# Optimization experiments

Measured on AMD Instinct MI355X. Metric: run time of the kernel, lower is better.

## Reference

```python
import jax, jax.numpy as jnp
import numpy as np

B, N, D = 64, 512, 256
IMG = 51  # hard-coded image-token prefix length from the original forward
EPS = 1e-8


def _l2norm(x):
    # matches torch.cosine_similarity eps clamping on each vector norm
    n = jnp.linalg.norm(x, axis=-1, keepdims=True)
    return x / jnp.maximum(n, EPS)


def setup_inputs() -> dict:
    key = jax.random.key(0)
    ks = jax.random.split(key, 10)
    s = 1.0 / np.sqrt(D)
    return {
        "input_1": jax.random.normal(ks[0], (B, N, D), jnp.float32),
        "input_2": jax.random.normal(ks[1], (B, N, D), jnp.float32),
        "attention_mask": jnp.ones((B, N), jnp.int32),  # unused by forward, kept for signature fidelity
        "noun_mask": jax.random.randint(ks[2], (B, N), 0, 2, jnp.int32),
        "w0": jax.random.uniform(ks[3], (D, D), jnp.float32, -s, s),
        "b0": jax.random.uniform(ks[4], (D,), jnp.float32, -s, s),
        "w1": jax.random.uniform(ks[5], (D, D), jnp.float32, -s, s),
        "b1": jax.random.uniform(ks[6], (D,), jnp.float32, -s, s),
        "wf": jax.random.uniform(ks[7], (D, D), jnp.float32, -s, s),
        "bf": jax.random.uniform(ks[8], (D,), jnp.float32, -s, s),
    }


def reference(input_1, input_2, attention_mask, noun_mask, w0, b0, w1, b1, wf, bf):
    img = _l2norm(input_2[:, :IMG, :])    # [B, 51, D]
    text = _l2norm(input_2[:, IMG:, :])   # [B, N-51, D]
    # cosine similarity via normalized matmul (no O(N*M*D) repeat blowup)
    sim = jnp.einsum('bid,btd->bit', img, text)            # [B, 51, N-51]
    nm = noun_mask[:, IMG:].astype(sim.dtype)[:, None, :]  # [B, 1, N-51]
    sim = sim * nm
    text_sim = jnp.einsum('bid,bjd->bij', text, text)      # [B, N-51, N-51]
    adj = jnp.zeros((B, N, N), input_2.dtype)
    adj = adj.at[:, :IMG, IMG:].set(sim)
    adj = adj.at[:, IMG:, :IMG].set(jnp.swapaxes(sim, 1, 2))
    adj = adj.at[:, IMG:, IMG:].set(text_sim)
    h = input_1
    for w, b in ((w0, b0), (w1, b1)):  # gcn_layer_num = 2; dropout is identity at eval
        h = jax.nn.relu(jnp.einsum('bnm,bmd->bnd', adj, h) @ w.T + b)
    return jax.nn.relu(h @ wf.T + bf)
```

## Files before the change

kernel.cpp:

```cpp
#include <hip/hip_runtime.h>
#include <math.h>

#define Bn   64
#define Nn   512
#define Dn   256
#define IMGn 51

typedef __attribute__((ext_vector_type(8))) short bf16x8;
typedef __attribute__((ext_vector_type(4))) float f32x4;
typedef __attribute__((ext_vector_type(4))) unsigned short u16x4;

__device__ inline unsigned short f2b(float f) {
    union { float f; unsigned u; } v; v.f = f;
    unsigned r = v.u + 0x7fffu + ((v.u >> 16) & 1u);
    return (unsigned short)(r >> 16);
}

__global__ __launch_bounds__(256) void k_prep(const float* __restrict__ in1,
                                              const float* __restrict__ in2,
                                              const float* __restrict__ w0,
                                              const float* __restrict__ w1,
                                              const float* __restrict__ wf,
                                              unsigned short* __restrict__ A0,
                                              unsigned short* __restrict__ T,
                                              unsigned short* __restrict__ w0b,
                                              unsigned short* __restrict__ w1b,
                                              unsigned short* __restrict__ wfb) {
    const int bid = blockIdx.x, tid = threadIdx.x;
    if (bid < 8192) {
        const int xcd = bid & 7, j = bid >> 3;
        const int b = xcd * 8 + (j >> 7), rb = j & 127;
        const int row = b * 512 + rb * 4 + (tid >> 6);
        const int lane = tid & 63;
        float4 v = ((const float4*)(in2 + (size_t)row * Dn))[lane];
        float ss = v.x * v.x + v.y * v.y + v.z * v.z + v.w * v.w;
#pragma unroll
        for (int m = 1; m < 64; m <<= 1) ss += __shfl_xor(ss, m);
        float inv = 1.0f / fmaxf(sqrtf(ss), 1e-8f);
        u16x4 o = { f2b(v.x*inv), f2b(v.y*inv), f2b(v.z*inv), f2b(v.w*inv) };
        ((u16x4*)(T + (size_t)row * Dn))[lane] = o;
    } else if (bid < 10240) {
        const int id2 = bid - 8192;
        const int xcd = id2 & 7, j = id2 >> 3;
        const int b = xcd * 8 + (j >> 5), jj = j & 31;
        int i = b * 32768 + jj * 1024 + tid;
#pragma unroll
        for (int q = 0; q < 4; ++q, i += 256) {
            float4 v = ((const float4*)in1)[i];
            u16x4 o = { f2b(v.x), f2b(v.y), f2b(v.z), f2b(v.w) };
            ((u16x4*)A0)[i] = o;
        }
    } else {
        const int b2 = bid - 10240;
        const float* src = (b2 < 64) ? w0 : (b2 < 128) ? w1 : wf;
        unsigned short* dst = (b2 < 64) ? w0b : (b2 < 128) ? w1b : wfb;
        const int i = (b2 & 63) * 256 + tid;
        float4 v = ((const float4*)src)[i];
        u16x4 o = { f2b(v.x), f2b(v.y), f2b(v.z), f2b(v.w) };
        ((u16x4*)dst)[i] = o;
    }
}

__device__ inline void stage128x32(const unsigned short* __restrict__ src, int ldk,
                                   char* ldsbase, int tid) {
    const int wave = tid >> 6, lane = tid & 63;
#pragma unroll
    for (int it = 0; it < 2; ++it) {
        const int chunk = wave * 128 + it * 64 + lane;
        const int row = chunk >> 2, s = chunk & 3;
        const char* g = (const char*)(src + (size_t)row * ldk) + ((s ^ ((row >> 1) & 3)) << 4);
        char* l = ldsbase + (size_t)(wave * 2048 + it * 1024);
        __builtin_amdgcn_global_load_lds((const __attribute__((address_space(1))) void*)g,
                                         (__attribute__((address_space(3))) void*)l,
                                         16, 0, 0);
    }
}

__device__ inline bf16x8 frag(const char* ldsbase, int row, int s) {
    return *(const bf16x8*)(ldsbase + row * 64 + ((s ^ ((row >> 1) & 3)) << 4));
}

__device__ inline void gemm_loop(const unsigned short* __restrict__ A,
                                 const unsigned short* __restrict__ Bt,
                                 int lda, int ldb, int NT, char* smem, int tid,
                                 int wr, int wc, int r16, int s, f32x4 (&acc)[4][4]) {
#pragma unroll
    for (int m = 0; m < 4; ++m)
#pragma unroll
        for (int n = 0; n < 4; ++n) acc[m][n] = (f32x4){0.f, 0.f, 0.f, 0.f};
    stage128x32(A,  lda, smem,        tid);
    stage128x32(Bt, ldb, smem + 8192, tid);
    __syncthreads();
    for (int t = 0; t < NT; ++t) {
        if (t + 1 < NT) {
            char* nb = smem + 17408 * ((t + 1) & 1);
            stage128x32(A  + (t + 1) * 32, lda, nb,        tid);
            stage128x32(Bt + (t + 1) * 32, ldb, nb + 8192, tid);
        }
        const char* cb = smem + 17408 * (t & 1);
        bf16x8 af[4], bv[4];
#pragma unroll
        for (int m = 0; m < 4; ++m) af[m] = frag(cb,        wr * 64 + m * 16 + r16, s);
#pragma unroll
        for (int n = 0; n < 4; ++n) bv[n] = frag(cb + 8192, wc * 64 + n * 16 + r16, s);
#pragma unroll
        for (int m = 0; m < 4; ++m)
#pragma unroll
            for (int n = 0; n < 4; ++n)
                acc[m][n] = __builtin_amdgcn_mfma_f32_16x16x32_bf16(af[m], bv[n], acc[m][n], 0, 0, 0);
        __syncthreads();
    }
}

__global__ __launch_bounds__(256, 4) void k_gt(const unsigned short* __restrict__ T_,
                                               const unsigned short* __restrict__ A0,
                                               const unsigned short* __restrict__ w0b,
                                               const int* __restrict__ noun,
                                               unsigned short* __restrict__ adj,
                                               unsigned short* __restrict__ Ut) {
    __shared__ char smem[34816];
    const int tid = threadIdx.x, lane = tid & 63, wave = tid >> 6;
    const int wr = wave >> 1, wc = wave & 1;
    const int r16 = lane & 15, s = lane >> 4;
    const int id = blockIdx.x, xcd = id & 7, gid = id >> 3;
    f32x4 acc[4][4];

    if (gid < 80) {
        const int b = xcd * 8 + (gid & 7);
        const int tile = gid >> 3;
        int ty_, tx_;
        if (tile < 4)      { ty_ = 0; tx_ = tile; }
        else if (tile < 7) { ty_ = 1; tx_ = tile - 3; }
        else if (tile < 9) { ty_ = 2; tx_ = tile - 5; }
        else               { ty_ = 3; tx_ = 3; }
        const unsigned short* Tb = T_ + (size_t)b * Nn * Dn;
        gemm_loop(Tb + (size_t)ty_ * 128 * Dn, Tb + (size_t)tx_ * 128 * Dn,
                  Dn, Dn, 8, smem, tid, wr, wc, r16, s, acc);
        const int row0 = ty_ * 128, col0 = tx_ * 128;
        const int* nm = noun + b * Nn;
        unsigned short* out = adj + (size_t)b * Nn * Nn;
        unsigned short* lt = (unsigned short*)smem;
        const int row = tid >> 1, h = tid & 1;
#pragma unroll
        for (int n = 0; n < 4; ++n) {
            const int cl = wc * 64 + n * 16 + r16;
            const int c  = col0 + cl;
            const float nmc = (c < IMGn) ? 0.f : (float)nm[c];
#pragma unroll
            for (int m = 0; m < 4; ++m)
#pragma unroll
                for (int i = 0; i < 4; ++i) {
                    const int rl = wr * 64 + m * 16 + s * 4 + i;
                    const int r  = row0 + rl;
                    float mask;
                    if (r < IMGn)      mask = nmc;
                    else if (c < IMGn) mask = (float)nm[r];
                    else               mask = 1.f;
                    lt[rl * 136 + cl] = f2b(acc[m][n][i] * mask);
                }
        }
        __syncthreads();
        {
            const bf16x8* srcv = (const bf16x8*)(lt + (size_t)row * 136 + h * 64);
            bf16x8* dstv = (bf16x8*)(out + (size_t)(row0 + row) * Nn + col0 + h * 64);
#pragma unroll
            for (int q = 0; q < 8; ++q) dstv[q] = srcv[q];
        }
        if (tx_ != ty_) {
            __syncthreads();
#pragma unroll
            for (int n = 0; n < 4; ++n) {
                const int cl = wc * 64 + n * 16 + r16;
                const int c  = col0 + cl;
                const float nmc = (c < IMGn) ? 0.f : (float)nm[c];
#pragma unroll
                for (int m = 0; m < 4; ++m)
#pragma unroll
                    for (int i = 0; i < 4; ++i) {
                        const int rl = wr * 64 + m * 16 + s * 4 + i;
                        const int r  = row0 + rl;
                        float mask;
                        if (r < IMGn)      mask = nmc;
                        else if (c < IMGn) mask = (float)nm[r];
                        else               mask = 1.f;
                        lt[cl * 136 + rl] = f2b(acc[m][n][i] * mask);
                    }
            }
            __syncthreads();
            const bf16x8* srcv = (const bf16x8*)(lt + (size_t)row * 136 + h * 64);
            bf16x8* dstv = (bf16x8*)(out + (size_t)(col0 + row) * Nn + row0 + h * 64);
#pragma unroll
            for (int q = 0; q < 8; ++q) dstv[q] = srcv[q];
        }
    } else {
        const int idx = xcd * 64 + (gid - 80);
        const int tx = idx & 1, ty = idx >> 1;
        gemm_loop(A0 + (size_t)ty * 128 * Dn, w0b + (size_t)tx * 128 * Dn,
                  Dn, Dn, 8, smem, tid, wr, wc, r16, s, acc);
        unsigned short* lt = (unsigned short*)smem;
#pragma unroll
        for (int n = 0; n < 4; ++n)
#pragma unroll
            for (int m = 0; m < 4; ++m)
#pragma unroll
                for (int i = 0; i < 4; ++i) {
                    const int ct = wc * 64 + n * 16 + r16;
                    const int rt = wr * 64 + m * 16 + s * 4 + i;
                    lt[ct * 136 + rt] = f2b(acc[m][n][i]);
                }
        __syncthreads();
        const size_t bb = ty >> 2;
        const int rl0 = (ty & 3) * 128, col0 = tx * 128;
        unsigned short* out = Ut + bb * ((size_t)Dn * Nn);
        const int ct = tid >> 1, h = tid & 1;
        const bf16x8* srcv = (const bf16x8*)(lt + (size_t)ct * 136 + h * 64);
        bf16x8* dstv = (bf16x8*)(out + (size_t)(col0 + ct) * Nn + rl0 + h * 64);
#pragma unroll
        for (int q = 0; q < 8; ++q) dstv[q] = srcv[q];
    }
}

__global__ __launch_bounds__(256, 4) void k_biash(const unsigned short* __restrict__ adj,
                                                  const unsigned short* __restrict__ Ut,
                                                  const float* __restrict__ bias,
                                                  unsigned short* __restrict__ H) {
    __shared__ char smem[34816];
    const int tid = threadIdx.x, lane = tid & 63, wave = tid >> 6;
    const int wr = wave >> 1, wc = wave & 1;
    const int r16 = lane & 15, s = lane >> 4;
    const int id = blockIdx.x, xcd = id & 7, gid = id >> 3;
    const int b = xcd * 8 + (gid >> 3);
    const int tile = gid & 7, tx = tile & 1, ty = tile >> 1;
    f32x4 acc[4][4];
    gemm_loop(adj + (size_t)b * Nn * Nn + (size_t)ty * 128 * Nn,
              Ut  + (size_t)b * Dn * Nn + (size_t)tx * 128 * Nn,
              Nn, Nn, 16, smem, tid, wr, wc, r16, s, acc);
    const int row0 = ty * 128, col0 = tx * 128;
    unsigned short* lt = (unsigned short*)smem;
#pragma unroll
    for (int n = 0; n < 4; ++n) {
        const int cl = wc * 64 + n * 16 + r16;
        const float bvv = bias[col0 + cl];
#pragma unroll
        for (int m = 0; m < 4; ++m)
#pragma unroll
            for (int i = 0; i < 4; ++i) {
                const int rl = wr * 64 + m * 16 + s * 4 + i;
                lt[rl * 136 + cl] = f2b(fmaxf(acc[m][n][i] + bvv, 0.f));
            }
    }
    __syncthreads();
    unsigned short* out = H + (size_t)b * Nn * Dn;
    const int row = tid >> 1, h = tid & 1;
    const bf16x8* srcv = (const bf16x8*)(lt + (size_t)row * 136 + h * 64);
    bf16x8* dstv = (bf16x8*)(out + (size_t)(row0 + row) * Dn + col0 + h * 64);
#pragma unroll
    for (int q = 0; q < 8; ++q) dstv[q] = srcv[q];
}

__global__ __launch_bounds__(256, 4) void k_trans(const unsigned short* __restrict__ Hin,
                                                  const unsigned short* __restrict__ Wb,
                                                  unsigned short* __restrict__ Ut) {
    __shared__ char smem[34816];
    const int tid = threadIdx.x, lane = tid & 63, wave = tid >> 6;
    const int wr = wave >> 1, wc = wave & 1;
    const int r16 = lane & 15, s = lane >> 4;
    const int id = blockIdx.x, xcd = id & 7;
    const int idx = xcd * 64 + (id >> 3);
    const int tx = idx & 1, ty = idx >> 1;
    f32x4 acc[4][4];
    gemm_loop(Hin + (size_t)ty * 128 * Dn, Wb + (size_t)tx * 128 * Dn,
              Dn, Dn, 8, smem, tid, wr, wc, r16, s, acc);
    unsigned short* lt = (unsigned short*)smem;
#pragma unroll
    for (int n = 0; n < 4; ++n)
#pragma unroll
        for (int m = 0; m < 4; ++m)
#pragma unroll
            for (int i = 0; i < 4; ++i) {
                const int ct = wc * 64 + n * 16 + r16;
                const int rt = wr * 64 + m * 16 + s * 4 + i;
                lt[ct * 136 + rt] = f2b(acc[m][n][i]);
            }
    __syncthreads();
    const size_t bb = ty >> 2;
    const int rl0 = (ty & 3) * 128, col0 = tx * 128;
    unsigned short* out = Ut + bb * ((size_t)Dn * Nn);
    const int ct = tid >> 1, h = tid & 1;
    const bf16x8* srcv = (const bf16x8*)(lt + (size_t)ct * 136 + h * 64);
    bf16x8* dstv = (bf16x8*)(out + (size_t)(col0 + ct) * Nn + rl0 + h * 64);
#pragma unroll
    for (int q = 0; q < 8; ++q) dstv[q] = srcv[q];
}

__global__ __launch_bounds__(256, 4) void k_final(const unsigned short* __restrict__ H2,
                                                  const unsigned short* __restrict__ wfb,
                                                  const float* __restrict__ bias,
                                                  float* __restrict__ out) {
    __shared__ char smem[34816];
    const int tid = threadIdx.x, lane = tid & 63, wave = tid >> 6;
    const int wr = wave >> 1, wc = wave & 1;
    const int r16 = lane & 15, s = lane >> 4;
    const int id = blockIdx.x, xcd = id & 7;
    const int idx = xcd * 64 + (id >> 3);
    const int tx = idx & 1, ty = idx >> 1;
    f32x4 acc[4][4];
    gemm_loop(H2 + (size_t)ty * 128 * Dn, wfb + (size_t)tx * 128 * Dn,
              Dn, Dn, 8, smem, tid, wr, wc, r16, s, acc);
    const int row0 = ty * 128, col0 = tx * 128;
    float* lt32 = (float*)smem;
    const int row = tid >> 1, h = tid & 1;
#pragma unroll
    for (int p = 0; p < 2; ++p) {
        if (p) __syncthreads();
        if (wc == p) {
#pragma unroll
            for (int n = 0; n < 4; ++n) {
                const int cll = n * 16 + r16;
                const float bvv = bias[col0 + p * 64 + cll];
#pragma unroll
                for (int m = 0; m < 4; ++m)
#pragma unroll
                    for (int i = 0; i < 4; ++i) {
                        const int rl = wr * 64 + m * 16 + s * 4 + i;
                        lt32[rl * 68 + cll] = fmaxf(acc[m][n][i] + bvv, 0.f);
                    }
            }
        }
        __syncthreads();
        const float4* srcv = (const float4*)(lt32 + (size_t)row * 68 + h * 32);
        float4* dstv = (float4*)(out + (size_t)(row0 + row) * Dn + col0 + p * 64 + h * 32);
#pragma unroll
        for (int q = 0; q < 8; ++q) dstv[q] = srcv[q];
    }
}

extern "C" void kernel_launch(void* const* d_in, const int* in_sizes, int n_in,
                              void* d_out, int out_size, void* d_ws, size_t ws_size,
                              hipStream_t stream) {
    const float* input_1 = (const float*)d_in[0];
    const float* input_2 = (const float*)d_in[1];
    const int*   noun    = (const int*)d_in[3];
    const float* w0 = (const float*)d_in[4];
    const float* b0 = (const float*)d_in[5];
    const float* w1 = (const float*)d_in[6];
    const float* b1 = (const float*)d_in[7];
    const float* wf = (const float*)d_in[8];
    const float* bf = (const float*)d_in[9];

    unsigned short* ws  = (unsigned short*)d_ws;
    unsigned short* T   = ws;
    unsigned short* A0  = ws +  8388608;
    unsigned short* adj = ws + 16777216;
    unsigned short* Ut  = ws + 33554432;
    unsigned short* H1  = ws + 41943040;
    unsigned short* H2  = ws + 50331648;
    unsigned short* w0b = ws + 58720256;
    unsigned short* w1b = w0b + 65536;
    unsigned short* wfb = w1b + 65536;

    dim3 blk(256);
    k_prep<<<10432, blk, 0, stream>>>(input_1, input_2, w0, w1, wf, A0, T, w0b, w1b, wfb);
    k_gt<<<1152, blk, 0, stream>>>(T, A0, w0b, noun, adj, Ut);
    k_biash<<<512, blk, 0, stream>>>(adj, Ut, b0, H1);
    k_trans<<<512, blk, 0, stream>>>(H1, w1b, Ut);
    k_biash<<<512, blk, 0, stream>>>(adj, Ut, b1, H2);
    k_final<<<512, blk, 0, stream>>>(H2, wfb, bf, (float*)d_out);
}
```

Measured before the change: 125.2 us.

## Halve GEMM output tile width to 128x64 to double grid size

Templates the GEMM loop on the number of N fragments and switches the biash, trans, final and the Ut part of k_gt from 128x128 to 128x64 output tiles, doubling block counts (512→1024, k_gt 1152→1664). It also shrinks LDS footprints and splits the k_gt adjacency epilogue into two 64-column passes so it fits 32KB, raising k_gt launch bounds to 5 blocks per CU. The aim is better CU fill on 256 CUs and more waves per CU to hide latency, at the cost of re-reading the A operand twice as often and lower MFMA reuse per LDS load.

```diff
diff --git a/kernel.cpp b/kernel.cpp
--- a/kernel.cpp
+++ b/kernel.cpp
@@ -67,8 +67,8 @@
 #pragma unroll
     for (int it = 0; it < 2; ++it) {
         const int chunk = wave * 128 + it * 64 + lane;
-        const int row = chunk >> 2, s = chunk & 3;
-        const char* g = (const char*)(src + (size_t)row * ldk) + ((s ^ ((row >> 1) & 3)) << 4);
+        const int row = chunk >> 2, sl = chunk & 3;
+        const char* g = (const char*)(src + (size_t)row * ldk) + ((sl ^ ((row >> 1) & 3)) << 4);
         char* l = ldsbase + (size_t)(wave * 2048 + it * 1024);
         __builtin_amdgcn_global_load_lds((const __attribute__((address_space(1))) void*)g,
                                          (__attribute__((address_space(3))) void*)l,
@@ -76,54 +76,69 @@
     }
 }
 
+__device__ inline void stage64x32(const unsigned short* __restrict__ src, int ldk,
+                                  char* ldsbase, int tid) {
+    const int wave = tid >> 6, lane = tid & 63;
+    const int chunk = wave * 64 + lane;
+    const int row = chunk >> 2, sl = chunk & 3;
+    const char* g = (const char*)(src + (size_t)row * ldk) + ((sl ^ ((row >> 1) & 3)) << 4);
+    char* l = ldsbase + (size_t)(wave * 1024);
+    __builtin_amdgcn_global_load_lds((const __attribute__((address_space(1))) void*)g,
+                                     (__attribute__((address_space(3))) void*)l,
+                                     16, 0, 0);
+}
+
 __device__ inline bf16x8 frag(const char* ldsbase, int row, int s) {
     return *(const bf16x8*)(ldsbase + row * 64 + ((s ^ ((row >> 1) & 3)) << 4));
 }
 
-__device__ inline void gemm_loop(const unsigned short* __restrict__ A,
-                                 const unsigned short* __restrict__ Bt,
-                                 int lda, int ldb, int NT, char* smem, int tid,
-                                 int wr, int wc, int r16, int s, f32x4 (&acc)[4][4]) {
+template<int NF>
+__device__ inline void gemm_loopT(const unsigned short* __restrict__ A,
+                                  const unsigned short* __restrict__ Bt,
+                                  int lda, int ldb, int NT, char* smem, int tid,
+                                  int wr, int wc, int r16, int s, f32x4 (&acc)[4][NF]) {
+    constexpr int SLOT = 8192 + NF * 2048;
 #pragma unroll
     for (int m = 0; m < 4; ++m)
 #pragma unroll
-        for (int n = 0; n < 4; ++n) acc[m][n] = (f32x4){0.f, 0.f, 0.f, 0.f};
-    stage128x32(A,  lda, smem,        tid);
-    stage128x32(Bt, ldb, smem + 8192, tid);
+        for (int n = 0; n < NF; ++n) acc[m][n] = (f32x4){0.f, 0.f, 0.f, 0.f};
+    stage128x32(A, lda, smem, tid);
+    if constexpr (NF == 4) stage128x32(Bt, ldb, smem + 8192, tid);
+    else                   stage64x32 (Bt, ldb, smem + 8192, tid);
     __syncthreads();
     for (int t = 0; t < NT; ++t) {
         if (t + 1 < NT) {
-            char* nb = smem + 17408 * ((t + 1) & 1);
-            stage128x32(A  + (t + 1) * 32, lda, nb,        tid);
-            stage128x32(Bt + (t + 1) * 32, ldb, nb + 8192, tid);
-        }
-        const char* cb = smem + 17408 * (t & 1);
-        bf16x8 af[4], bv[4];
-#pragma unroll
-        for (int m = 0; m < 4; ++m) af[m] = frag(cb,        wr * 64 + m * 16 + r16, s);
-#pragma unroll
-        for (int n = 0; n < 4; ++n) bv[n] = frag(cb + 8192, wc * 64 + n * 16 + r16, s);
+            char* nb = smem + SLOT * ((t + 1) & 1);
+            stage128x32(A + (t + 1) * 32, lda, nb, tid);
+            if constexpr (NF == 4) stage128x32(Bt + (t + 1) * 32, ldb, nb + 8192, tid);
+            else                   stage64x32 (Bt + (t + 1) * 32, ldb, nb + 8192, tid);
+        }
+        const char* cb = smem + SLOT * (t & 1);
+        bf16x8 af[4], bv[NF];
+#pragma unroll
+        for (int m = 0; m < 4; ++m) af[m] = frag(cb, wr * 64 + m * 16 + r16, s);
+#pragma unroll
+        for (int n = 0; n < NF; ++n) bv[n] = frag(cb + 8192, wc * (NF * 16) + n * 16 + r16, s);
 #pragma unroll
         for (int m = 0; m < 4; ++m)
 #pragma unroll
-            for (int n = 0; n < 4; ++n)
+            for (int n = 0; n < NF; ++n)
                 acc[m][n] = __builtin_amdgcn_mfma_f32_16x16x32_bf16(af[m], bv[n], acc[m][n], 0, 0, 0);
         __syncthreads();
     }
 }
 
-__global__ __launch_bounds__(256, 4) void k_gt(const unsigned short* __restrict__ T_,
+__global__ __launch_bounds__(256, 5) void k_gt(const unsigned short* __restrict__ T_,
                                                const unsigned short* __restrict__ A0,
                                                const unsigned short* __restrict__ w0b,
                                                const int* __restrict__ noun,
                                                unsigned short* __restrict__ adj,
                                                unsigned short* __restrict__ Ut) {
-    __shared__ char smem[34816];
+    __shared__ char smem[32768];
     const int tid = threadIdx.x, lane = tid & 63, wave = tid >> 6;
     const int wr = wave >> 1, wc = wave & 1;
     const int r16 = lane & 15, s = lane >> 4;
     const int id = blockIdx.x, xcd = id & 7, gid = id >> 3;
-    f32x4 acc[4][4];
 
     if (gid < 80) {
         const int b = xcd * 8 + (gid & 7);
@@ -134,89 +149,100 @@
         else if (tile < 9) { ty_ = 2; tx_ = tile - 5; }
         else               { ty_ = 3; tx_ = 3; }
         const unsigned short* Tb = T_ + (size_t)b * Nn * Dn;
-        gemm_loop(Tb + (size_t)ty_ * 128 * Dn, Tb + (size_t)tx_ * 128 * Dn,
-                  Dn, Dn, 8, smem, tid, wr, wc, r16, s, acc);
+        f32x4 acc[4][4];
+        gemm_loopT<4>(Tb + (size_t)ty_ * 128 * Dn, Tb + (size_t)tx_ * 128 * Dn,
+                      Dn, Dn, 8, smem, tid, wr, wc, r16, s, acc);
         const int row0 = ty_ * 128, col0 = tx_ * 128;
         const int* nm = noun + b * Nn;
         unsigned short* out = adj + (size_t)b * Nn * Nn;
         unsigned short* lt = (unsigned short*)smem;
         const int row = tid >> 1, h = tid & 1;
 #pragma unroll
-        for (int n = 0; n < 4; ++n) {
-            const int cl = wc * 64 + n * 16 + r16;
-            const int c  = col0 + cl;
-            const float nmc = (c < IMGn) ? 0.f : (float)nm[c];
+        for (int p = 0; p < 2; ++p) {
+            if (p) __syncthreads();
+            if (wc == p) {
+#pragma unroll
+                for (int n = 0; n < 4; ++n) {
+                    const int cll = n * 16 + r16;
+                    const int c  = col0 + p * 64 + cll;
+                    const float nmc = (c < IMGn) ? 0.f : (float)nm[c];
+#pragma unroll
+                    for (int m = 0; m < 4; ++m)
+#pragma unroll
+                        for (int i = 0; i < 4; ++i) {
+                            const int rl = wr * 64 + m * 16 + s * 4 + i;
+                            const int r  = row0 + rl;
+                            float mask;
+                            if (r < IMGn)      mask = nmc;
+                            else if (c < IMGn) mask = (float)nm[r];
+                            else               mask = 1.f;
+                            lt[rl * 68 + cll] = f2b(acc[m][n][i] * mask);
+                        }
+                }
+            }
+            __syncthreads();
+            const bf16x8* srcv = (const bf16x8*)(lt + (size_t)row * 68 + h * 32);
+            bf16x8* dstv = (bf16x8*)(out + (size_t)(row0 + row) * Nn + col0 + p * 64 + h * 32);
+#pragma unroll
+            for (int q = 0; q < 4; ++q) dstv[q] = srcv[q];
+        }
+        if (tx_ != ty_) {
+#pragma unroll
+            for (int p = 0; p < 2; ++p) {
+                __syncthreads();
+                if (wr == p) {
+#pragma unroll
+                    for (int n = 0; n < 4; ++n) {
+                        const int cl = wc * 64 + n * 16 + r16;
+                        const int c  = col0 + cl;
+                        const float nmc = (c < IMGn) ? 0.f : (float)nm[c];
+#pragma unroll
+                        for (int m = 0; m < 4; ++m)
+#pragma unroll
+                            for (int i = 0; i < 4; ++i) {
+                                const int rll = m * 16 + s * 4 + i;
+                                const int r   = row0 + p * 64 + rll;
+                                float mask;
+                                if (r < IMGn)      mask = nmc;
+                                else if (c < IMGn) mask = (float)nm[r];
+                                else               mask = 1.f;
+                                lt[cl * 68 + rll] = f2b(acc[m][n][i] * mask);
+                            }
+                    }
+                }
+                __syncthreads();
+                const bf16x8* srcv = (const bf16x8*)(lt + (size_t)row * 68 + h * 32);
+                bf16x8* dstv = (bf16x8*)(out + (size_t)(col0 + row) * Nn + row0 + p * 64 + h * 32);
+#pragma unroll
+                for (int q = 0; q < 4; ++q) dstv[q] = srcv[q];
+            }
+        }
+    } else {
+        const int idx = xcd * 128 + (gid - 80);
+        const int tx = idx & 3, ty = idx >> 2;
+        f32x4 acc[4][2];
+        gemm_loopT<2>(A0 + (size_t)ty * 128 * Dn, w0b + (size_t)tx * 64 * Dn,
+                      Dn, Dn, 8, smem, tid, wr, wc, r16, s, acc);
+        unsigned short* lt = (unsigned short*)smem;
+#pragma unroll
+        for (int n = 0; n < 2; ++n)
 #pragma unroll
             for (int m = 0; m < 4; ++m)
 #pragma unroll
                 for (int i = 0; i < 4; ++i) {
-                    const int rl = wr * 64 + m * 16 + s * 4 + i;
-                    const int r  = row0 + rl;
-                    float mask;
-                    if (r < IMGn)      mask = nmc;
-                    else if (c < IMGn) mask = (float)nm[r];
-                    else               mask = 1.f;
-                    lt[rl * 136 + cl] = f2b(acc[m][n][i] * mask);
-                }
-        }
-        __syncthreads();
-        {
-            const bf16x8* srcv = (const bf16x8*)(lt + (size_t)row * 136 + h * 64);
-            bf16x8* dstv = (bf16x8*)(out + (size_t)(row0 + row) * Nn + col0 + h * 64);
-#pragma unroll
-            for (int q = 0; q < 8; ++q) dstv[q] = srcv[q];
-        }
-        if (tx_ != ty_) {
-            __syncthreads();
-#pragma unroll
-            for (int n = 0; n < 4; ++n) {
-                const int cl = wc * 64 + n * 16 + r16;
-                const int c  = col0 + cl;
-                const float nmc = (c < IMGn) ? 0.f : (float)nm[c];
-#pragma unroll
-                for (int m = 0; m < 4; ++m)
-#pragma unroll
-                    for (int i = 0; i < 4; ++i) {
-                        const int rl = wr * 64 + m * 16 + s * 4 + i;
-                        const int r  = row0 + rl;
-                        float mask;
-                        if (r < IMGn)      mask = nmc;
-                        else if (c < IMGn) mask = (float)nm[r];
-                        else               mask = 1.f;
-                        lt[cl * 136 + rl] = f2b(acc[m][n][i] * mask);
-                    }
-            }
-            __syncthreads();
-            const bf16x8* srcv = (const bf16x8*)(lt + (size_t)row * 136 + h * 64);
-            bf16x8* dstv = (bf16x8*)(out + (size_t)(col0 + row) * Nn + row0 + h * 64);
-#pragma unroll
-            for (int q = 0; q < 8; ++q) dstv[q] = srcv[q];
-        }
-    } else {
-        const int idx = xcd * 64 + (gid - 80);
-        const int tx = idx & 1, ty = idx >> 1;
-        gemm_loop(A0 + (size_t)ty * 128 * Dn, w0b + (size_t)tx * 128 * Dn,
-                  Dn, Dn, 8, smem, tid, wr, wc, r16, s, acc);
-        unsigned short* lt = (unsigned short*)smem;
-#pragma unroll
-        for (int n = 0; n < 4; ++n)
-#pragma unroll
-            for (int m = 0; m < 4; ++m)
-#pragma unroll
-                for (int i = 0; i < 4; ++i) {
-                    const int ct = wc * 64 + n * 16 + r16;
+                    const int ct = wc * 32 + n * 16 + r16;
                     const int rt = wr * 64 + m * 16 + s * 4 + i;
                     lt[ct * 136 + rt] = f2b(acc[m][n][i]);
                 }
         __syncthreads();
         const size_t bb = ty >> 2;
-        const int rl0 = (ty & 3) * 128, col0 = tx * 128;
+        const int rl0 = (ty & 3) * 128, col0 = tx * 64;
         unsigned short* out = Ut + bb * ((size_t)Dn * Nn);
-        const int ct = tid >> 1, h = tid & 1;
-        const bf16x8* srcv = (const bf16x8*)(lt + (size_t)ct * 136 + h * 64);
-        bf16x8* dstv = (bf16x8*)(out + (size_t)(col0 + ct) * Nn + rl0 + h * 64);
-#pragma unroll
-        for (int q = 0; q < 8; ++q) dstv[q] = srcv[q];
+        const int ctr = tid >> 2, q4 = tid & 3;
+        const bf16x8* srcv = (const bf16x8*)(lt + (size_t)ctr * 136 + q4 * 32);
+        bf16x8* dstv = (bf16x8*)(out + (size_t)(col0 + ctr) * Nn + rl0 + q4 * 32);
+#pragma unroll
+        for (int q = 0; q < 4; ++q) dstv[q] = srcv[q];
     }
 }
 
@@ -224,90 +250,90 @@
                                                   const unsigned short* __restrict__ Ut,
                                                   const float* __restrict__ bias,
                                                   unsigned short* __restrict__ H) {
-    __shared__ char smem[34816];
+    __shared__ char smem[24576];
     const int tid = threadIdx.x, lane = tid & 63, wave = tid >> 6;
     const int wr = wave >> 1, wc = wave & 1;
     const int r16 = lane & 15, s = lane >> 4;
     const int id = blockIdx.x, xcd = id & 7, gid = id >> 3;
-    const int b = xcd * 8 + (gid >> 3);
-    const int tile = gid & 7, tx = tile & 1, ty = tile >> 1;
-    f32x4 acc[4][4];
-    gemm_loop(adj + (size_t)b * Nn * Nn + (size_t)ty * 128 * Nn,
-              Ut  + (size_t)b * Dn * Nn + (size_t)tx * 128 * Nn,
-              Nn, Nn, 16, smem, tid, wr, wc, r16, s, acc);
-    const int row0 = ty * 128, col0 = tx * 128;
+    const int b = xcd * 8 + (gid >> 4);
+    const int tile = gid & 15, tx = tile & 3, ty = tile >> 2;
+    f32x4 acc[4][2];
+    gemm_loopT<2>(adj + (size_t)b * Nn * Nn + (size_t)ty * 128 * Nn,
+                  Ut  + (size_t)b * Dn * Nn + (size_t)tx * 64 * Nn,
+                  Nn, Nn, 16, smem, tid, wr, wc, r16, s, acc);
+    const int row0 = ty * 128, col0 = tx * 64;
     unsigned short* lt = (unsigned short*)smem;
 #pragma unroll
-    for (int n = 0; n < 4; ++n) {
-        const int cl = wc * 64 + n * 16 + r16;
+    for (int n = 0; n < 2; ++n) {
+        const int cl = wc * 32 + n * 16 + r16;
         const float bvv = bias[col0 + cl];
 #pragma unroll
         for (int m = 0; m < 4; ++m)
 #pragma unroll
             for (int i = 0; i < 4; ++i) {
                 const int rl = wr * 64 + m * 16 + s * 4 + i;
-                lt[rl * 136 + cl] = f2b(fmaxf(acc[m][n][i] + bvv, 0.f));
+                lt[rl * 68 + cl] = f2b(fmaxf(acc[m][n][i] + bvv, 0.f));
             }
     }
     __syncthreads();
     unsigned short* out = H + (size_t)b * Nn * Dn;
     const int row = tid >> 1, h = tid & 1;
-    const bf16x8* srcv = (const bf16x8*)(lt + (size_t)row * 136 + h * 64);
-    bf16x8* dstv = (bf16x8*)(out + (size_t)(row0 + row) * Dn + col0 + h * 64);
-#pragma unroll
-    for (int q = 0; q < 8; ++q) dstv[q] = srcv[q];
+    const bf16x8* srcv = (const bf16x8*)(lt + (size_t)row * 68 + h * 32);
+    bf16x8* dstv = (bf16x8*)(out + (size_t)(row0 + row) * Dn + col0 + h * 32);
+#pragma unroll
+    for (int q = 0; q < 4; ++q) dstv[q] = srcv[q];
 }
 
 __global__ __launch_bounds__(256, 4) void k_trans(const unsigned short* __restrict__ Hin,
                                                   const unsigned short* __restrict__ Wb,
                                                   unsigned short* __restrict__ Ut) {
-    __shared__ char smem[34816];
+    __shared__ char smem[24576];
     const int tid = threadIdx.x, lane = tid & 63, wave = tid >> 6;
     const int wr = wave >> 1, wc = wave & 1;
     const int r16 = lane & 15, s = lane >> 4;
     const int id = blockIdx.x, xcd = id & 7;
-    const int idx = xcd * 64 + (id >> 3);
-    const int tx = idx & 1, ty = idx >> 1;
-    f32x4 acc[4][4];
-    gemm_loop(Hin + (size_t)ty * 128 * Dn, Wb + (size_t)tx * 128 * Dn,
-              Dn, Dn, 8, smem, tid, wr, wc, r16, s, acc);
+    const int idx = xcd * 128 + (id >> 3);
+    const int tx = idx & 3, ty = idx >> 2;
+    f32x4 acc[4][2];
+    gemm_loopT<2>(Hin + (size_t)ty * 128 * Dn, Wb + (size_t)tx * 64 * Dn,
+                  Dn, Dn, 8, smem, tid, wr, wc, r16, s, acc);
     unsigned short* lt = (unsigned short*)smem;
 #pragma unroll
-    for (int n = 0; n < 4; ++n)
+    for (int n = 0; n < 2; ++n)
 #pragma unroll
         for (int m = 0; m < 4; ++m)
 #pragma unroll
             for (int i = 0; i < 4; ++i) {
-                const int ct = wc * 64 + n * 16 + r16;
+                const int ct = wc * 32 + n * 16 + r16;
                 const int rt = wr * 64 + m * 16 + s * 4 + i;
                 lt[ct * 136 + rt] = f2b(acc[m][n][i]);
             }
     __syncthreads();
     const size_t bb = ty >> 2;
-    const int rl0 = (ty & 3) * 128, col0 = tx * 128;
+    const int rl0 = (ty & 3) * 128, col0 = tx * 64;
     unsigned short* out = Ut + bb * ((size_t)Dn * Nn);
-    const int ct = tid >> 1, h = tid & 1;
-    const bf16x8* srcv = (const bf16x8*)(lt + (size_t)ct * 136 + h * 64);
-    bf16x8* dstv = (bf16x8*)(out + (size_t)(col0 + ct) * Nn + rl0 + h * 64);
-#pragma unroll
-    for (int q = 0; q < 8; ++q) dstv[q] = srcv[q];
+    const int ctr = tid >> 2, q4 = tid & 3;
+    const bf16x8* srcv = (const bf16x8*)(lt + (size_t)ctr * 136 + q4 * 32);
+    bf16x8* dstv = (bf16x8*)(out + (size_t)(col0 + ctr) * Nn + rl0 + q4 * 32);
+#pragma unroll
+    for (int q = 0; q < 4; ++q) dstv[q] = srcv[q];
 }
 
 __global__ __launch_bounds__(256, 4) void k_final(const unsigned short* __restrict__ H2,
                                                   const unsigned short* __restrict__ wfb,
                                                   const float* __restrict__ bias,
                                                   float* __restrict__ out) {
-    __shared__ char smem[34816];
+    __shared__ char smem[24576];
     const int tid = threadIdx.x, lane = tid & 63, wave = tid >> 6;
     const int wr = wave >> 1, wc = wave & 1;
     const int r16 = lane & 15, s = lane >> 4;
     const int id = blockIdx.x, xcd = id & 7;
-    const int idx = xcd * 64 + (id >> 3);
-    const int tx = idx & 1, ty = idx >> 1;
-    f32x4 acc[4][4];
-    gemm_loop(H2 + (size_t)ty * 128 * Dn, wfb + (size_t)tx * 128 * Dn,
-              Dn, Dn, 8, smem, tid, wr, wc, r16, s, acc);
-    const int row0 = ty * 128, col0 = tx * 128;
+    const int idx = xcd * 128 + (id >> 3);
+    const int tx = idx & 3, ty = idx >> 2;
+    f32x4 acc[4][2];
+    gemm_loopT<2>(H2 + (size_t)ty * 128 * Dn, wfb + (size_t)tx * 64 * Dn,
+                  Dn, Dn, 8, smem, tid, wr, wc, r16, s, acc);
+    const int row0 = ty * 128, col0 = tx * 64;
     float* lt32 = (float*)smem;
     const int row = tid >> 1, h = tid & 1;
 #pragma unroll
@@ -315,23 +341,23 @@
         if (p) __syncthreads();
         if (wc == p) {
 #pragma unroll
-            for (int n = 0; n < 4; ++n) {
+            for (int n = 0; n < 2; ++n) {
                 const int cll = n * 16 + r16;
-                const float bvv = bias[col0 + p * 64 + cll];
+                const float bvv = bias[col0 + p * 32 + cll];
 #pragma unroll
                 for (int m = 0; m < 4; ++m)
 #pragma unroll
                     for (int i = 0; i < 4; ++i) {
                         const int rl = wr * 64 + m * 16 + s * 4 + i;
-                        lt32[rl * 68 + cll] = fmaxf(acc[m][n][i] + bvv, 0.f);
+                        lt32[rl * 36 + cll] = fmaxf(acc[m][n][i] + bvv, 0.f);
                     }
             }
         }
         __syncthreads();
-        const float4* srcv = (const float4*)(lt32 + (size_t)row * 68 + h * 32);
-        float4* dstv = (float4*)(out + (size_t)(row0 + row) * Dn + col0 + p * 64 + h * 32);
-#pragma unroll
-        for (int q = 0; q < 8; ++q) dstv[q] = srcv[q];
+        const float4* srcv = (const float4*)(lt32 + (size_t)row * 36 + h * 16);
+        float4* dstv = (float4*)(out + (size_t)(row0 + row) * Dn + col0 + p * 32 + h * 16);
+#pragma unroll
+        for (int q = 0; q < 4; ++q) dstv[q] = srcv[q];
     }
 }
 
@@ -361,9 +387,9 @@
 
     dim3 blk(256);
     k_prep<<<10432, blk, 0, stream>>>(input_1, input_2, w0, w1, wf, A0, T, w0b, w1b, wfb);
-    k_gt<<<1152, blk, 0, stream>>>(T, A0, w0b, noun, adj, Ut);
-    k_biash<<<512, blk, 0, stream>>>(adj, Ut, b0, H1);
-    k_trans<<<512, blk, 0, stream>>>(H1, w1b, Ut);
-    k_biash<<<512, blk, 0, stream>>>(adj, Ut, b1, H2);
-    k_final<<<512, blk, 0, stream>>>(H2, wfb, bf, (float*)d_out);
-}
+    k_gt<<<1664, blk, 0, stream>>>(T, A0, w0b, noun, adj, Ut);
+    k_biash<<<1024, blk, 0, stream>>>(adj, Ut, b0, H1);
+    k_trans<<<1024, blk, 0, stream>>>(H1, w1b, Ut);
+    k_biash<<<1024, blk, 0, stream>>>(adj, Ut, b1, H2);
+    k_final<<<1024, blk, 0, stream>>>(H2, wfb, bf, (float*)d_out);
+}
```

Measured after the change: 140.3 us. 12.1% more time.
